# Kernel tuning notes

Hardware: AMD Instinct MI355X
Metric: run time of the kernel (lower is better)

Reference implementation:

```python
import jax, jax.numpy as jnp
import numpy as np

B, S, D = 2, 4096, 1024
H, DK, DV = 4, 128, 256          # head_k_dim, head_v_dim
KD, VD = H * DK, H * DV          # key_dim=512, value_dim=1024
RANK = 16                        # gate_low_rank_dim
GLN = 16.0                       # gate_logit_normalizer
EPS = 1e-5
C = 64                           # chunk size
NC = S // C


def setup_inputs() -> dict:
    key = jax.random.key(0)
    ks = jax.random.split(key, 9)
    w = lambda k, shape: (jax.random.normal(k, shape, jnp.float32) * 0.02)
    return {
        "x": jax.random.normal(ks[0], (B, S, D), jnp.float32),
        "Wq": w(ks[1], (D, KD)),
        "Wk": w(ks[2], (D, KD)),
        "Wv": w(ks[3], (D, VD)),
        "Wgk1": w(ks[4], (D, RANK)),
        "Wgk2": w(ks[5], (RANK, KD)),
        "bgk": jnp.zeros((KD,), jnp.float32),
        "Wg": w(ks[6], (D, VD)),
        "Wo": w(ks[7], (VD, D)),
        "norm_w": jnp.ones((DV,), jnp.float32),
    }


def _gla_chunk(q, k, v, gk):
    """Chunkwise gated linear attention. q,k,gk: [B,S,H,DK]; v: [B,S,H,DV]."""
    qc = q.reshape(B, NC, C, H, DK)
    kc = k.reshape(B, NC, C, H, DK)
    vc = v.reshape(B, NC, C, H, DV)
    gc = gk.reshape(B, NC, C, H, DK)
    gcum = jnp.cumsum(gc, axis=2)                       # inclusive within-chunk cumsum (<= 0)
    g_last = gcum[:, :, -1]                             # [B,NC,H,DK]
    q_t = qc * jnp.exp(gcum)                            # q decayed forward
    k_inv = kc * jnp.exp(-gcum)                         # for intra-chunk scores
    k_dec = kc * jnp.exp(g_last[:, :, None] - gcum)     # for state update (bounded)
    # intra-chunk causal scores
    A = jnp.einsum('bnthk,bnshk->bnhts', q_t, k_inv)    # [B,NC,H,C,C]
    mask = jnp.tril(jnp.ones((C, C), bool))
    A = jnp.where(mask, A, 0.0)
    o_intra = jnp.einsum('bnhts,bnshv->bnthv', A, vc)   # [B,NC,C,H,DV]
    # per-chunk state contribution
    kv = jnp.einsum('bnthk,bnthv->bnhkv', k_dec, vc)    # [B,NC,H,DK,DV]

    def step(state, inp):
        q_tc, gl, kvc = inp                             # [B,C,H,DK], [B,H,DK], [B,H,DK,DV]
        o_inter = jnp.einsum('bthk,bhkv->bthv', q_tc, state)
        state = state * jnp.exp(gl)[..., None] + kvc
        return state, o_inter

    xs = (jnp.swapaxes(q_t, 0, 1), jnp.swapaxes(g_last, 0, 1), jnp.swapaxes(kv, 0, 1))
    init = jnp.zeros((B, H, DK, DV), q.dtype)
    _, o_inter = jax.lax.scan(step, init, xs)           # [NC,B,C,H,DV]
    o = o_intra + jnp.swapaxes(o_inter, 0, 1)
    return o.reshape(B, S, H, DV)


def reference(x, Wq, Wk, Wv, Wgk1, Wgk2, bgk, Wg, Wo, norm_w):
    scale = DK ** -0.5
    q = (x @ Wq).reshape(B, S, H, DK) * scale
    k = (x @ Wk).reshape(B, S, H, DK)
    v = (x @ Wv).reshape(B, S, H, DV)
    gk = (jax.nn.log_sigmoid((x @ Wgk1) @ Wgk2 + bgk) / GLN).reshape(B, S, H, DK)
    o = _gla_chunk(q, k, v, gk)                          # [B,S,H,DV]
    # fused RMSNorm + swish gate (per-head norm over DV)
    g = (x @ Wg).reshape(B, S, H, DV)
    o = o * jax.lax.rsqrt(jnp.mean(o * o, axis=-1, keepdims=True) + EPS) * norm_w
    o = o * (g * jax.nn.sigmoid(g))
    return o.reshape(B, S, VD) @ Wo
```

## Files before the change

kernel.cpp:

```cpp
#include <hip/hip_runtime.h>

typedef __bf16 bf16_t;
typedef __bf16 bf16x8 __attribute__((ext_vector_type(8)));
typedef float  f32x4  __attribute__((ext_vector_type(4)));

#define MFMA16(a,b,c) __builtin_amdgcn_mfma_f32_16x16x32_bf16((a),(b),(c),0,0,0)

#define SCALE_Q 0.08838834764831845f

#define GLOBAL_LOAD_LDS16(gptr, lptr)                                          \
  __builtin_amdgcn_global_load_lds(                                            \
      (const __attribute__((address_space(1))) void*)(gptr),                   \
      (__attribute__((address_space(3))) void*)(lptr), 16, 0, 0)

__global__ __launch_bounds__(256) void k_convert(const void* __restrict__ src,
                                                 const unsigned int* __restrict__ nwp,
                                                 bf16_t* __restrict__ dst, int n) {
  bool isf32 = (nwp[0] == 0x3F800000u);
  int g = blockIdx.x * 256 + threadIdx.x;
  int i = g * 8;
  if (i >= n) return;
  if (isf32) {
    const float4* s = (const float4*)src;
    float4 a = s[g * 2], b = s[g * 2 + 1];
    bf16x8 o;
    o[0] = (bf16_t)a.x; o[1] = (bf16_t)a.y; o[2] = (bf16_t)a.z; o[3] = (bf16_t)a.w;
    o[4] = (bf16_t)b.x; o[5] = (bf16_t)b.y; o[6] = (bf16_t)b.z; o[7] = (bf16_t)b.w;
    *(bf16x8*)(dst + i) = o;
  } else {
    *(bf16x8*)(dst + i) = ((const bf16x8*)src)[g];
  }
}

struct ConvSrcs {
  const void *wq, *wk, *wv, *wg, *wo, *gk1, *gk2, *bgk, *nw;
};
__device__ __forceinline__ void convT_tile(const void* src, bf16_t* dst,
                                           int Ccols, int bx, int by,
                                           bool isf32, bf16_t (*t)[33]) {
  int tx = threadIdx.x & 31, ty = threadIdx.x >> 5;
  int r0 = by * 32, c0 = bx * 32;
#pragma unroll
  for (int i = 0; i < 4; i++) {
    int r = r0 + ty + i * 8, cc = c0 + tx;
    float v = isf32 ? ((const float*)src)[(size_t)r * Ccols + cc]
                    : (float)((const bf16_t*)src)[(size_t)r * Ccols + cc];
    t[ty + i * 8][tx] = (bf16_t)v;
  }
  __syncthreads();
#pragma unroll
  for (int i = 0; i < 4; i++) {
    int cc = c0 + ty + i * 8;
    dst[(size_t)cc * 1024 + r0 + tx] = t[tx][ty + i * 8];
  }
}
__device__ __forceinline__ void conv_straight(const void* src, bf16_t* dst,
                                              int base_blk, int n, bool isf32) {
  int g = (blockIdx.x - base_blk) * 256 + threadIdx.x;
  int i = g * 8;
  if (i >= n) return;
  if (isf32) {
    const float4* s = (const float4*)src;
    float4 a = s[g * 2], b = s[g * 2 + 1];
    bf16x8 o;
    o[0] = (bf16_t)a.x; o[1] = (bf16_t)a.y; o[2] = (bf16_t)a.z; o[3] = (bf16_t)a.w;
    o[4] = (bf16_t)b.x; o[5] = (bf16_t)b.y; o[6] = (bf16_t)b.z; o[7] = (bf16_t)b.w;
    *(bf16x8*)(dst + i) = o;
  } else {
    *(bf16x8*)(dst + i) = ((const bf16x8*)src)[g];
  }
}
__global__ __launch_bounds__(256) void k_convW(ConvSrcs s,
                                               const unsigned int* __restrict__ nwp,
                                               bf16_t* __restrict__ tWcat,
                                               bf16_t* __restrict__ tWo,
                                               bf16_t* __restrict__ cWgk1,
                                               bf16_t* __restrict__ cWgk2,
                                               bf16_t* __restrict__ cbgk,
                                               bf16_t* __restrict__ cnw) {
  __shared__ bf16_t t[32][33];
  bool isf32 = (nwp[0] == 0x3F800000u);
  int blk = blockIdx.x;
  if (blk < 512) {
    convT_tile(s.wq, tWcat, 512, blk & 15, blk >> 4, isf32, t);
  } else if (blk < 1024) {
    int b2 = blk - 512;
    convT_tile(s.wk, tWcat + (size_t)512 * 1024, 512, b2 & 15, b2 >> 4, isf32, t);
  } else if (blk < 2048) {
    int b2 = blk - 1024;
    convT_tile(s.wv, tWcat + (size_t)1024 * 1024, 1024, b2 & 31, b2 >> 5, isf32, t);
  } else if (blk < 3072) {
    int b2 = blk - 2048;
    convT_tile(s.wg, tWcat + (size_t)2048 * 1024, 1024, b2 & 31, b2 >> 5, isf32, t);
  } else if (blk < 4096) {
    int b2 = blk - 3072;
    convT_tile(s.wo, tWo, 1024, b2 & 31, b2 >> 5, isf32, t);
  } else if (blk < 4104) {
    conv_straight(s.gk1, cWgk1, 4096, 16384, isf32);
  } else if (blk < 4108) {
    conv_straight(s.gk2, cWgk2, 4104, 8192, isf32);
  } else if (blk == 4108) {
    conv_straight(s.bgk, cbgk, 4108, 512, isf32);
  } else {
    conv_straight(s.nw, cnw, 4109, 256, isf32);
  }
}

__global__ __launch_bounds__(256) void k_gk1(const bf16_t* __restrict__ x,
                                             const bf16_t* __restrict__ W1,
                                             float* __restrict__ tmp) {
  int wave = threadIdx.x >> 6, lane = threadIdx.x & 63;
  int m = blockIdx.x * 4 + wave;
  const bf16_t* xr = x + (size_t)m * 1024;
  float p[16];
#pragma unroll
  for (int n = 0; n < 16; n++) p[n] = 0.f;
  for (int kk = 0; kk < 16; kk++) {
    int k = kk * 64 + lane;
    float xv = (float)xr[k];
    bf16x8 w0 = *(const bf16x8*)(W1 + k * 16);
    bf16x8 w1 = *(const bf16x8*)(W1 + k * 16 + 8);
#pragma unroll
    for (int j = 0; j < 8; j++) {
      p[j]     += xv * (float)w0[j];
      p[8 + j] += xv * (float)w1[j];
    }
  }
#pragma unroll
  for (int off = 1; off < 64; off <<= 1) {
#pragma unroll
    for (int n = 0; n < 16; n++) p[n] += __shfl_xor(p[n], off, 64);
  }
#pragma unroll
  for (int n = 0; n < 16; n++)
    if (lane == n) tmp[(size_t)m * 16 + n] = p[n];
}

__global__ __launch_bounds__(256) void k_gk2(const float* __restrict__ tmp,
                                             const bf16_t* __restrict__ W2,
                                             const bf16_t* __restrict__ bgk,
                                             float* __restrict__ gcum) {
  int g = blockIdx.x * 256 + threadIdx.x;
  int m = g >> 6;
  int n0 = (g & 63) * 8;
  float acc[8];
#pragma unroll
  for (int j = 0; j < 8; j++) acc[j] = 0.f;
  for (int k = 0; k < 16; k++) {
    float tv = tmp[(size_t)m * 16 + k];
    bf16x8 w = *(const bf16x8*)(W2 + k * 512 + n0);
#pragma unroll
    for (int j = 0; j < 8; j++) acc[j] += tv * (float)w[j];
  }
  int b = m >> 12, s = m & 4095;
  int h = n0 >> 7, dk0 = n0 & 127;
  float* dst = gcum + (((size_t)(b * 4 + h) * 4096 + s) * 128 + dk0);
#pragma unroll
  for (int j = 0; j < 8; j++) {
    float z = acc[j] + (float)bgk[n0 + j];
    float lg = -__logf(1.f + __expf(-z)) * (1.f / 16.f);
    dst[j] = fmaxf(lg, -4.0f);
  }
}

__global__ __launch_bounds__(128) void k_cumsum(float* __restrict__ gcum,
                                                float* __restrict__ glast) {
  int blk = blockIdx.x;
  int dk = threadIdx.x;
  float* base = gcum + (size_t)blk * 8192;
  float run = 0.f;
  for (int t = 0; t < 64; t++) {
    run += base[t * 128 + dk];
    base[t * 128 + dk] = run;
  }
  glast[(size_t)blk * 128 + dk] = run;
}

__global__ __launch_bounds__(256, 4) void k_gemm(const bf16_t* __restrict__ Ag,
                                              const bf16_t* __restrict__ Bt,
                                              int mode,
                                              const float* __restrict__ gcum,
                                              const float* __restrict__ glast,
                                              bf16_t* __restrict__ qt,
                                              bf16_t* __restrict__ kinv,
                                              bf16_t* __restrict__ kdec,
                                              bf16_t* __restrict__ vr,
                                              bf16_t* __restrict__ gmat,
                                              float* __restrict__ fout) {
  __shared__ __attribute__((aligned(16))) bf16_t As[2 * 128 * 32];
  __shared__ __attribute__((aligned(16))) bf16_t Bs[2 * 128 * 32];
  int tid = threadIdx.x;
  int wave = tid >> 6, lane = tid & 63, quad = lane >> 4, c = lane & 15;
  int m0 = blockIdx.y * 128, n0 = blockIdx.x * 128;
  int wm = (wave >> 1) * 64, wn = (wave & 1) * 64;
  int r0s = wave * 32 + (lane >> 2);
  int r1s = r0s + 16;
  int s = lane & 3;
  int f0 = (s - (r0s >> 1)) & 3;
  int f1 = (s - (r1s >> 1)) & 3;
  const bf16_t* a0 = Ag + (size_t)(m0 + r0s) * 1024 + f0 * 8;
  const bf16_t* a1 = Ag + (size_t)(m0 + r1s) * 1024 + f1 * 8;
  const bf16_t* b0 = Bt + (size_t)(n0 + r0s) * 1024 + f0 * 8;
  const bf16_t* b1 = Bt + (size_t)(n0 + r1s) * 1024 + f1 * 8;
  bf16_t* lA = As + wave * 1024;
  bf16_t* lB = Bs + wave * 1024;
  int raOff[4], rbOff[4];
#pragma unroll
  for (int t4 = 0; t4 < 4; t4++) {
    int ra = wm + t4 * 16 + c;
    raOff[t4] = ra * 32 + (((quad + (ra >> 1)) & 3) * 8);
    int rb = wn + t4 * 16 + c;
    rbOff[t4] = rb * 32 + (((quad + (rb >> 1)) & 3) * 8);
  }
  GLOBAL_LOAD_LDS16(a0, lA);
  GLOBAL_LOAD_LDS16(a1, lA + 512);
  GLOBAL_LOAD_LDS16(b0, lB);
  GLOBAL_LOAD_LDS16(b1, lB + 512);
  f32x4 acc[4][4] = {};
  for (int k0 = 0; k0 < 1024; k0 += 32) {
    __syncthreads();
    int cur = (k0 >> 5) & 1;
    int nxtoff = (cur ^ 1) * 4096;
    if (k0 + 32 < 1024) {
      GLOBAL_LOAD_LDS16(a0 + k0 + 32, lA + nxtoff);
      GLOBAL_LOAD_LDS16(a1 + k0 + 32, lA + nxtoff + 512);
      GLOBAL_LOAD_LDS16(b0 + k0 + 32, lB + nxtoff);
      GLOBAL_LOAD_LDS16(b1 + k0 + 32, lB + nxtoff + 512);
    }
    int curoff = cur * 4096;
    bf16x8 af[4], bfr[4];
#pragma unroll
    for (int t4 = 0; t4 < 4; t4++) af[t4] = *(const bf16x8*)(As + curoff + raOff[t4]);
#pragma unroll
    for (int t4 = 0; t4 < 4; t4++) bfr[t4] = *(const bf16x8*)(Bs + curoff + rbOff[t4]);
#pragma unroll
    for (int mt = 0; mt < 4; mt++)
#pragma unroll
      for (int nt = 0; nt < 4; nt++)
        acc[mt][nt] = MFMA16(af[mt], bfr[nt], acc[mt][nt]);
  }
#pragma unroll
  for (int mt = 0; mt < 4; mt++)
#pragma unroll
    for (int nt = 0; nt < 4; nt++)
#pragma unroll
      for (int r = 0; r < 4; r++) {
        int m = m0 + wm + mt * 16 + quad * 4 + r;
        int n = n0 + wn + nt * 16 + c;
        float v = acc[mt][nt][r];
        if (mode == 1) {
          fout[(size_t)m * 1024 + n] = v;
        } else if (n0 < 512) {
          int b = m >> 12, ss = m & 4095, h = n >> 7, dk = n & 127;
          size_t idx = ((size_t)(b * 4 + h) * 4096 + ss) * 128 + dk;
          qt[idx] = (bf16_t)(v * SCALE_Q * __expf(gcum[idx]));
        } else if (n0 < 1024) {
          int nk = n - 512;
          int b = m >> 12, ss = m & 4095, h = nk >> 7, dk = nk & 127;
          size_t idx = ((size_t)(b * 4 + h) * 4096 + ss) * 128 + dk;
          float gc = gcum[idx];
          float gl = glast[((size_t)(b * 4 + h) * 64 + (ss >> 6)) * 128 + dk];
          kinv[idx] = (bf16_t)(v * __expf(fminf(-gc, 30.f)));
          kdec[idx] = (bf16_t)(v * __expf(gl - gc));
        } else if (n0 < 2048) {
          int nv = n - 1024;
          int b = m >> 12, ss = m & 4095, h = nv >> 8, dv = nv & 255;
          vr[((size_t)(b * 4 + h) * 4096 + ss) * 256 + dv] = (bf16_t)v;
        } else {
          gmat[(size_t)m * 1024 + (n - 2048)] = (bf16_t)v;
        }
      }
}

__global__ __launch_bounds__(256) void k_attA(const bf16_t* __restrict__ qt,
                                              const bf16_t* __restrict__ kinv,
                                              bf16_t* __restrict__ Aout) {
  int blk = blockIdx.x;
  size_t cb = (size_t)blk * 8192;
  int tid = threadIdx.x, wave = tid >> 6, lane = tid & 63;
  int quad = lane >> 4, c = lane & 15;
  f32x4 acc[4] = {};
  for (int kk = 0; kk < 128; kk += 32) {
    bf16x8 a = *(const bf16x8*)(qt + cb + (size_t)(wave * 16 + c) * 128 + kk + quad * 8);
#pragma unroll
    for (int nt = 0; nt < 4; nt++) {
      bf16x8 bb = *(const bf16x8*)(kinv + cb + (size_t)(nt * 16 + c) * 128 + kk + quad * 8);
      acc[nt] = MFMA16(a, bb, acc[nt]);
    }
  }
#pragma unroll
  for (int nt = 0; nt < 4; nt++)
#pragma unroll
    for (int r = 0; r < 4; r++) {
      int row = wave * 16 + quad * 4 + r, col = nt * 16 + c;
      Aout[(size_t)blk * 4096 + row * 64 + col] =
          (bf16_t)(col <= row ? acc[nt][r] : 0.f);
    }
}

__global__ __launch_bounds__(256, 3) void k_kv(const bf16_t* __restrict__ kdec,
                                            const bf16_t* __restrict__ vr,
                                            bf16_t* __restrict__ kv) {
  int blk = blockIdx.x;
  __shared__ __attribute__((aligned(16))) bf16_t ls_kd[64 * 128];
  __shared__ __attribute__((aligned(16))) bf16_t ls_v[64 * 256];
  int tid = threadIdx.x, wave = tid >> 6, lane = tid & 63;
  int quad = lane >> 4, c = lane & 15;
  size_t cb = (size_t)blk * 8192;
  size_t cv = (size_t)blk * 16384;
  size_t sb = (size_t)blk * 32768;
#pragma unroll
  for (int j = 0; j < 4; j++) {
    int idx = tid + j * 256;
    int row = idx >> 4, col = (idx & 15) * 8;
    *(bf16x8*)&ls_kd[row * 128 + col] = *(const bf16x8*)(kdec + cb + (size_t)row * 128 + col);
  }
#pragma unroll
  for (int j = 0; j < 8; j++) {
    int idx = tid + j * 256;
    int row = idx >> 5, col = (idx & 31) * 8;
    *(bf16x8*)&ls_v[row * 256 + col] = *(const bf16x8*)(vr + cv + (size_t)row * 256 + col);
  }
  __syncthreads();
  int kbase = (wave >> 1) * 64;
  for (int pos = 0; pos < 2; pos++) {
    int dvbase = (wave & 1) * 64 + pos * 128;
    f32x4 acc[4][4] = {};
    for (int kk = 0; kk < 64; kk += 32) {
      bf16x8 a[4], bb[4];
#pragma unroll
      for (int mt = 0; mt < 4; mt++)
#pragma unroll
        for (int j = 0; j < 8; j++)
          a[mt][j] = ls_kd[(kk + quad * 8 + j) * 128 + kbase + mt * 16 + c];
#pragma unroll
      for (int nt = 0; nt < 4; nt++)
#pragma unroll
        for (int j = 0; j < 8; j++)
          bb[nt][j] = ls_v[(kk + quad * 8 + j) * 256 + dvbase + nt * 16 + c];
#pragma unroll
      for (int mt = 0; mt < 4; mt++)
#pragma unroll
        for (int nt = 0; nt < 4; nt++)
          acc[mt][nt] = MFMA16(a[mt], bb[nt], acc[mt][nt]);
    }
#pragma unroll
    for (int mt = 0; mt < 4; mt++)
#pragma unroll
      for (int nt = 0; nt < 4; nt++)
#pragma unroll
        for (int r = 0; r < 4; r++) {
          int kg = kbase + mt * 16 + quad * 4 + r;
          int dg = dvbase + nt * 16 + c;
          kv[sb + (size_t)kg * 256 + dg] = (bf16_t)acc[mt][nt][r];
        }
  }
}

__global__ __launch_bounds__(256) void k_scan2(bf16_t* __restrict__ states,
                                               const float* __restrict__ glast) {
  int g = blockIdx.x * 256 + threadIdx.x;
  int bh = g >> 15;
  int idx = g & 32767;
  int kg = idx >> 8;
  bf16_t* p = states + (size_t)bh * 64 * 32768 + idx;
  const float* gl = glast + (size_t)bh * 64 * 128 + kg;
  float carry = 0.f;
#pragma unroll 4
  for (int n = 0; n < 64; n++) {
    float kvv = (float)p[(size_t)n * 32768];
    float e = __expf(gl[n * 128]);
    p[(size_t)n * 32768] = (bf16_t)carry;
    carry = carry * e + kvv;
  }
}

__global__ __launch_bounds__(256, 4) void k_o(const bf16_t* __restrict__ qt,
                                           const bf16_t* __restrict__ Amat,
                                           const bf16_t* __restrict__ vr,
                                           const bf16_t* __restrict__ states,
                                           const bf16_t* __restrict__ gmat,
                                           const bf16_t* __restrict__ normw,
                                           bf16_t* __restrict__ ob) {
  int blk = blockIdx.x;
  int bh = blk >> 6, n = blk & 63, b = bh >> 2, h = bh & 3;
  __shared__ __attribute__((aligned(16))) bf16_t ls[64 * 256];
  __shared__ __attribute__((aligned(16))) float lred[64][4];
  int tid = threadIdx.x, wave = tid >> 6, lane = tid & 63;
  int quad = lane >> 4, c = lane & 15;
  size_t cb = (size_t)blk * 8192;
  size_t cv = (size_t)blk * 16384;
  size_t sb = (size_t)blk * 32768;
  f32x4 acc[4][4] = {};
  for (int half = 0; half < 2; half++) {
    __syncthreads();
#pragma unroll
    for (int i = 0; i < 8; i++) {
      int idx = tid + i * 256;
      int row = idx >> 5, col = (idx & 31) * 8;
      *(bf16x8*)&ls[row * 256 + col] =
          *(const bf16x8*)(states + sb + (size_t)(half * 64 + row) * 256 + col);
    }
    __syncthreads();
    for (int kk2 = 0; kk2 < 2; kk2++) {
      int kl = kk2 * 32, kg = half * 64 + kl;
      bf16x8 a[4], bb[4];
#pragma unroll
      for (int mt = 0; mt < 4; mt++)
        a[mt] = *(const bf16x8*)(qt + cb + (size_t)(mt * 16 + c) * 128 + kg + quad * 8);
#pragma unroll
      for (int nt = 0; nt < 4; nt++)
#pragma unroll
        for (int j = 0; j < 8; j++)
          bb[nt][j] = ls[(kl + quad * 8 + j) * 256 + wave * 64 + nt * 16 + c];
#pragma unroll
      for (int mt = 0; mt < 4; mt++)
#pragma unroll
        for (int nt = 0; nt < 4; nt++)
          acc[mt][nt] = MFMA16(a[mt], bb[nt], acc[mt][nt]);
    }
  }
  __syncthreads();
#pragma unroll
  for (int i = 0; i < 8; i++) {
    int idx = tid + i * 256;
    int row = idx >> 5, col = (idx & 31) * 8;
    *(bf16x8*)&ls[row * 256 + col] =
        *(const bf16x8*)(vr + cv + (size_t)row * 256 + col);
  }
  __syncthreads();
  for (int kk = 0; kk < 64; kk += 32) {
    bf16x8 a[4], bb[4];
#pragma unroll
    for (int mt = 0; mt < 4; mt++)
      a[mt] = *(const bf16x8*)(Amat + (size_t)blk * 4096 + (size_t)(mt * 16 + c) * 64 + kk + quad * 8);
#pragma unroll
    for (int nt = 0; nt < 4; nt++)
#pragma unroll
      for (int j = 0; j < 8; j++)
        bb[nt][j] = ls[(kk + quad * 8 + j) * 256 + wave * 64 + nt * 16 + c];
#pragma unroll
    for (int mt = 0; mt < 4; mt++)
#pragma unroll
      for (int nt = 0; nt < 4; nt++)
        acc[mt][nt] = MFMA16(a[mt], bb[nt], acc[mt][nt]);
  }
  float p[4][4];
#pragma unroll
  for (int mt = 0; mt < 4; mt++)
#pragma unroll
    for (int r = 0; r < 4; r++) {
      float s = 0.f;
#pragma unroll
      for (int nt = 0; nt < 4; nt++) s += acc[mt][nt][r] * acc[mt][nt][r];
      p[mt][r] = s;
    }
#pragma unroll
  for (int off = 1; off < 16; off <<= 1) {
#pragma unroll
    for (int mt = 0; mt < 4; mt++)
#pragma unroll
      for (int r = 0; r < 4; r++) p[mt][r] += __shfl_xor(p[mt][r], off, 64);
  }
  if (c == 0) {
#pragma unroll
    for (int mt = 0; mt < 4; mt++)
#pragma unroll
      for (int r = 0; r < 4; r++) lred[mt * 16 + quad * 4 + r][wave] = p[mt][r];
  }
  __syncthreads();
#pragma unroll
  for (int mt = 0; mt < 4; mt++)
#pragma unroll
    for (int r = 0; r < 4; r++) {
      int row = mt * 16 + quad * 4 + r;
      float tot = lred[row][0] + lred[row][1] + lred[row][2] + lred[row][3];
      float rs = rsqrtf(tot * (1.f / 256.f) + 1e-5f);
      int sg = n * 64 + row;
      size_t gb = ((size_t)(b * 4096 + sg)) * 1024 + h * 256;
#pragma unroll
      for (int nt = 0; nt < 4; nt++) {
        int dv = wave * 64 + nt * 16 + c;
        float ov = acc[mt][nt][r] * rs * (float)normw[dv];
        float gv = (float)gmat[gb + dv];
        ov *= gv / (1.f + __expf(-gv));
        ob[gb + dv] = (bf16_t)ov;
      }
    }
}

extern "C" void kernel_launch(void* const* d_in, const int* in_sizes, int n_in,
                              void* d_out, int out_size, void* d_ws, size_t ws_size,
                              hipStream_t stream) {
  (void)in_sizes; (void)n_in; (void)out_size; (void)ws_size;
  const unsigned int* nw_oracle = (const unsigned int*)d_in[9];

  char* ws = (char*)d_ws;
  size_t off = 0;
  auto alloc = [&](size_t bytes) -> void* {
    void* p = ws + off;
    off += (bytes + 255) & ~(size_t)255;
    return p;
  };
  bf16_t* states = (bf16_t*)alloc((size_t)512 * 32768 * 2);
  bf16_t* cx     = states;
  float*  glast  = (float*) alloc((size_t)8 * 64 * 128 * 4);
  float*  tmp    = (float*) alloc((size_t)8192 * 16 * 4);
  float*  gcum   = (float*) alloc((size_t)8 * 4096 * 128 * 4);
  bf16_t* ob     = (bf16_t*)gcum;
  bf16_t* qt     = (bf16_t*)alloc((size_t)8 * 4096 * 128 * 2);
  bf16_t* kinv   = (bf16_t*)alloc((size_t)8 * 4096 * 128 * 2);
  bf16_t* kdec   = (bf16_t*)alloc((size_t)8 * 4096 * 128 * 2);
  bf16_t* vr     = (bf16_t*)alloc((size_t)8 * 4096 * 256 * 2);
  bf16_t* gmat   = (bf16_t*)alloc((size_t)8192 * 1024 * 2);
  bf16_t* Amat   = (bf16_t*)alloc((size_t)512 * 4096 * 2);
  bf16_t* tWcat  = (bf16_t*)alloc((size_t)3072 * 1024 * 2);
  bf16_t* cWgk1  = (bf16_t*)alloc((size_t)1024 * 16 * 2);
  bf16_t* cWgk2  = (bf16_t*)alloc((size_t)16 * 512 * 2);
  bf16_t* cbgk   = (bf16_t*)alloc((size_t)512 * 2);
  bf16_t* tWo    = (bf16_t*)alloc((size_t)1024 * 1024 * 2);
  bf16_t* cnw    = (bf16_t*)alloc((size_t)256 * 2);

  k_convert<<<4096, 256, 0, stream>>>(d_in[0], nw_oracle, cx, 8192 * 1024);
  ConvSrcs cs{d_in[1], d_in[2], d_in[3], d_in[7], d_in[8],
              d_in[4], d_in[5], d_in[6], d_in[9]};
  k_convW<<<4110, 256, 0, stream>>>(cs, nw_oracle, tWcat, tWo,
                                    cWgk1, cWgk2, cbgk, cnw);

  k_gk1<<<2048, 256, 0, stream>>>(cx, cWgk1, tmp);
  k_gk2<<<2048, 256, 0, stream>>>(tmp, cWgk2, cbgk, gcum);
  k_cumsum<<<512, 128, 0, stream>>>(gcum, glast);
  k_gemm<<<dim3(24, 64), 256, 0, stream>>>(cx, tWcat, 0, gcum, glast,
                                           qt, kinv, kdec, vr, gmat, nullptr);
  k_attA<<<512, 256, 0, stream>>>(qt, kinv, Amat);
  k_kv<<<512, 256, 0, stream>>>(kdec, vr, states);
  k_scan2<<<1024, 256, 0, stream>>>(states, glast);
  k_o<<<512, 256, 0, stream>>>(qt, Amat, vr, states, gmat, cnw, ob);
  k_gemm<<<dim3(8, 64), 256, 0, stream>>>(ob, tWo, 1, nullptr, nullptr,
                                          nullptr, nullptr, nullptr, nullptr, nullptr,
                                          (float*)d_out);
}
```

Measured before the change: 343.2 us.

## Rewrite projection GEMMs with larger tiles, 512 threads, XOR-swizzled LDS and grid swizzle

Replaces the 128x128, 256-thread GEMM with a templated kernel that uses 256x256 (or 128x256) tiles, 8 waves, a K-step of 64 with XOR-swizzled LDS, and explicit vmcnt waits with barriers for double buffering. It also remaps the block index for L2 locality and raises wave priority during MFMA. The aim is more data reuse per LDS load and fewer global loads per FLOP. In exchange it needs up to 128KB of dynamic shared memory and launches fewer blocks (384 and 256), which may underfill the CUs.

```diff
diff --git a/kernel.cpp b/kernel.cpp
--- a/kernel.cpp
+++ b/kernel.cpp
@@ -12,6 +12,9 @@
   __builtin_amdgcn_global_load_lds(                                            \
       (const __attribute__((address_space(1))) void*)(gptr),                   \
       (__attribute__((address_space(3))) void*)(lptr), 16, 0, 0)
+
+#define SBAR   __builtin_amdgcn_s_barrier()
+#define SCHEDB __builtin_amdgcn_sched_barrier(0)
 
 __global__ __launch_bounds__(256) void k_convert(const void* __restrict__ src,
                                                  const unsigned int* __restrict__ nwp,
@@ -176,98 +179,134 @@
   glast[(size_t)blk * 128 + dk] = run;
 }
 
-__global__ __launch_bounds__(256, 4) void k_gemm(const bf16_t* __restrict__ Ag,
-                                              const bf16_t* __restrict__ Bt,
-                                              int mode,
-                                              const float* __restrict__ gcum,
-                                              const float* __restrict__ glast,
-                                              bf16_t* __restrict__ qt,
-                                              bf16_t* __restrict__ kinv,
-                                              bf16_t* __restrict__ kdec,
-                                              bf16_t* __restrict__ vr,
-                                              bf16_t* __restrict__ gmat,
-                                              float* __restrict__ fout) {
-  __shared__ __attribute__((aligned(16))) bf16_t As[2 * 128 * 32];
-  __shared__ __attribute__((aligned(16))) bf16_t Bs[2 * 128 * 32];
+template <int BM, int BN, int NBN, int MODE>
+__global__ __launch_bounds__(512, 2) void k_gemm2(
+    const bf16_t* __restrict__ Ag, const bf16_t* __restrict__ Bt,
+    const float* __restrict__ gcum, const float* __restrict__ glast,
+    bf16_t* __restrict__ qt, bf16_t* __restrict__ kinv,
+    bf16_t* __restrict__ kdec, bf16_t* __restrict__ vr,
+    bf16_t* __restrict__ gmat, float* __restrict__ fout) {
+  constexpr int MT = BM / 2 / 16;
+  constexpr int ALDS = BM * 64;
+  constexpr int BLDS = BN * 64;
+  constexpr int NT = 16;
+  extern __shared__ __attribute__((aligned(16))) bf16_t sm[];
+  bf16_t* As = sm;
+  bf16_t* Bs = sm + 2 * ALDS;
+
   int tid = threadIdx.x;
-  int wave = tid >> 6, lane = tid & 63, quad = lane >> 4, c = lane & 15;
-  int m0 = blockIdx.y * 128, n0 = blockIdx.x * 128;
-  int wm = (wave >> 1) * 64, wn = (wave & 1) * 64;
-  int r0s = wave * 32 + (lane >> 2);
-  int r1s = r0s + 16;
-  int s = lane & 3;
-  int f0 = (s - (r0s >> 1)) & 3;
-  int f1 = (s - (r1s >> 1)) & 3;
-  const bf16_t* a0 = Ag + (size_t)(m0 + r0s) * 1024 + f0 * 8;
-  const bf16_t* a1 = Ag + (size_t)(m0 + r1s) * 1024 + f1 * 8;
-  const bf16_t* b0 = Bt + (size_t)(n0 + r0s) * 1024 + f0 * 8;
-  const bf16_t* b1 = Bt + (size_t)(n0 + r1s) * 1024 + f1 * 8;
-  bf16_t* lA = As + wave * 1024;
-  bf16_t* lB = Bs + wave * 1024;
-  int raOff[4], rbOff[4];
-#pragma unroll
-  for (int t4 = 0; t4 < 4; t4++) {
-    int ra = wm + t4 * 16 + c;
-    raOff[t4] = ra * 32 + (((quad + (ra >> 1)) & 3) * 8);
-    int rb = wn + t4 * 16 + c;
-    rbOff[t4] = rb * 32 + (((quad + (rb >> 1)) & 3) * 8);
-  }
-  GLOBAL_LOAD_LDS16(a0, lA);
-  GLOBAL_LOAD_LDS16(a1, lA + 512);
-  GLOBAL_LOAD_LDS16(b0, lB);
-  GLOBAL_LOAD_LDS16(b1, lB + 512);
-  f32x4 acc[4][4] = {};
-  for (int k0 = 0; k0 < 1024; k0 += 32) {
-    __syncthreads();
-    int cur = (k0 >> 5) & 1;
-    int nxtoff = (cur ^ 1) * 4096;
-    if (k0 + 32 < 1024) {
-      GLOBAL_LOAD_LDS16(a0 + k0 + 32, lA + nxtoff);
-      GLOBAL_LOAD_LDS16(a1 + k0 + 32, lA + nxtoff + 512);
-      GLOBAL_LOAD_LDS16(b0 + k0 + 32, lB + nxtoff);
-      GLOBAL_LOAD_LDS16(b1 + k0 + 32, lB + nxtoff + 512);
-    }
-    int curoff = cur * 4096;
-    bf16x8 af[4], bfr[4];
-#pragma unroll
-    for (int t4 = 0; t4 < 4; t4++) af[t4] = *(const bf16x8*)(As + curoff + raOff[t4]);
-#pragma unroll
-    for (int t4 = 0; t4 < 4; t4++) bfr[t4] = *(const bf16x8*)(Bs + curoff + rbOff[t4]);
-#pragma unroll
-    for (int mt = 0; mt < 4; mt++)
+  int w = tid >> 6, lane = tid & 63;
+  int WM = w >> 2, WN = w & 3;
+  int quad = lane >> 4, c = lane & 15;
+
+  int nblk = gridDim.x;
+  int bid = blockIdx.x;
+  int swz = (bid & 7) * (nblk >> 3) + (bid >> 3);
+  int bm = swz / NBN, bn = swz % NBN;
+  int m0 = bm * BM, n0 = bn * BN;
+
+  int srow = w * 8 + (lane >> 3);
+  int scol = ((lane & 7) ^ (lane >> 3)) * 8;
+  const bf16_t* aBase = Ag + (size_t)(m0 + srow) * 1024 + scol;
+  const bf16_t* bBase = Bt + (size_t)(n0 + srow) * 1024 + scol;
+
+  auto stage = [&](int t, int buf) {
+    int kof = t * 64;
+#pragma unroll
+    for (int j = 0; j < BM / 64; j++)
+      GLOBAL_LOAD_LDS16(aBase + (size_t)j * 64 * 1024 + kof,
+                        As + buf * ALDS + j * 4096 + w * 512);
+#pragma unroll
+    for (int j = 0; j < BN / 64; j++)
+      GLOBAL_LOAD_LDS16(bBase + (size_t)j * 64 * 1024 + kof,
+                        Bs + buf * BLDS + j * 4096 + w * 512);
+  };
+
+  int sx = c & 7;
+  int aRowOff[MT], bRowOff[4];
+#pragma unroll
+  for (int mt = 0; mt < MT; mt++) aRowOff[mt] = (WM * (BM / 2) + mt * 16 + c) * 64;
+#pragma unroll
+  for (int nt = 0; nt < 4; nt++) bRowOff[nt] = (WN * 64 + nt * 16 + c) * 64;
+
+  f32x4 acc[MT][4] = {};
+
+  stage(0, 0);
+  stage(1, 1);
+
+  auto compute = [&](int buf) {
+#pragma unroll
+    for (int ks = 0; ks < 2; ks++) {
+      int so = (((ks << 2) | quad) ^ sx) << 3;
+      bf16x8 bfr[4];
 #pragma unroll
       for (int nt = 0; nt < 4; nt++)
-        acc[mt][nt] = MFMA16(af[mt], bfr[nt], acc[mt][nt]);
-  }
-#pragma unroll
-  for (int mt = 0; mt < 4; mt++)
+        bfr[nt] = *(const bf16x8*)(Bs + buf * BLDS + bRowOff[nt] + so);
+#pragma unroll
+      for (int mt = 0; mt < MT; mt++) {
+        bf16x8 af = *(const bf16x8*)(As + buf * ALDS + aRowOff[mt] + so);
+#pragma unroll
+        for (int nt = 0; nt < 4; nt++)
+          acc[mt][nt] = MFMA16(af, bfr[nt], acc[mt][nt]);
+      }
+    }
+  };
+
+#pragma unroll 2
+  for (int t = 0; t < NT; t++) {
+    if (t < NT - 1) {
+      if constexpr (BM == 256)
+        asm volatile("s_waitcnt vmcnt(8)" ::: "memory");
+      else
+        asm volatile("s_waitcnt vmcnt(6)" ::: "memory");
+    } else {
+      asm volatile("s_waitcnt vmcnt(0)" ::: "memory");
+    }
+    SCHEDB;
+    SBAR;
+    SCHEDB;
+    __builtin_amdgcn_s_setprio(1);
+    compute(t & 1);
+    __builtin_amdgcn_s_setprio(0);
+    SCHEDB;
+    SBAR;
+    SCHEDB;
+    if (t + 2 < NT) stage(t + 2, t & 1);
+  }
+
+  int mwb = m0 + WM * (BM / 2);
+  int nwb = n0 + WN * 64;
+#pragma unroll
+  for (int mt = 0; mt < MT; mt++)
 #pragma unroll
     for (int nt = 0; nt < 4; nt++)
 #pragma unroll
       for (int r = 0; r < 4; r++) {
-        int m = m0 + wm + mt * 16 + quad * 4 + r;
-        int n = n0 + wn + nt * 16 + c;
+        int m = mwb + mt * 16 + quad * 4 + r;
+        int n = nwb + nt * 16 + c;
         float v = acc[mt][nt][r];
-        if (mode == 1) {
+        if constexpr (MODE == 1) {
           fout[(size_t)m * 1024 + n] = v;
-        } else if (n0 < 512) {
-          int b = m >> 12, ss = m & 4095, h = n >> 7, dk = n & 127;
-          size_t idx = ((size_t)(b * 4 + h) * 4096 + ss) * 128 + dk;
-          qt[idx] = (bf16_t)(v * SCALE_Q * __expf(gcum[idx]));
-        } else if (n0 < 1024) {
-          int nk = n - 512;
-          int b = m >> 12, ss = m & 4095, h = nk >> 7, dk = nk & 127;
-          size_t idx = ((size_t)(b * 4 + h) * 4096 + ss) * 128 + dk;
-          float gc = gcum[idx];
-          float gl = glast[((size_t)(b * 4 + h) * 64 + (ss >> 6)) * 128 + dk];
-          kinv[idx] = (bf16_t)(v * __expf(fminf(-gc, 30.f)));
-          kdec[idx] = (bf16_t)(v * __expf(gl - gc));
-        } else if (n0 < 2048) {
-          int nv = n - 1024;
-          int b = m >> 12, ss = m & 4095, h = nv >> 8, dv = nv & 255;
-          vr[((size_t)(b * 4 + h) * 4096 + ss) * 256 + dv] = (bf16_t)v;
         } else {
-          gmat[(size_t)m * 1024 + (n - 2048)] = (bf16_t)v;
+          if (n0 < 512) {
+            int b = m >> 12, ss = m & 4095, h = n >> 7, dk = n & 127;
+            size_t idx = ((size_t)(b * 4 + h) * 4096 + ss) * 128 + dk;
+            qt[idx] = (bf16_t)(v * SCALE_Q * __expf(gcum[idx]));
+          } else if (n0 < 1024) {
+            int nk = n - 512;
+            int b = m >> 12, ss = m & 4095, h = nk >> 7, dk = nk & 127;
+            size_t idx = ((size_t)(b * 4 + h) * 4096 + ss) * 128 + dk;
+            float gc = gcum[idx];
+            float gl = glast[((size_t)(b * 4 + h) * 64 + (ss >> 6)) * 128 + dk];
+            kinv[idx] = (bf16_t)(v * __expf(fminf(-gc, 30.f)));
+            kdec[idx] = (bf16_t)(v * __expf(gl - gc));
+          } else if (n0 < 2048) {
+            int nv = n - 1024;
+            int b = m >> 12, ss = m & 4095, h = nv >> 8, dv = nv & 255;
+            vr[((size_t)(b * 4 + h) * 4096 + ss) * 256 + dv] = (bf16_t)v;
+          } else {
+            gmat[(size_t)m * 1024 + (n - 2048)] = (bf16_t)v;
+          }
         }
       }
 }
@@ -494,6 +533,15 @@
                               hipStream_t stream) {
   (void)in_sizes; (void)n_in; (void)out_size; (void)ws_size;
   const unsigned int* nw_oracle = (const unsigned int*)d_in[9];
+
+  static int attr_done = 0;
+  if (!attr_done) {
+    (void)hipFuncSetAttribute((const void*)&k_gemm2<256, 256, 12, 0>,
+                              hipFuncAttributeMaxDynamicSharedMemorySize, 131072);
+    (void)hipFuncSetAttribute((const void*)&k_gemm2<128, 256, 4, 1>,
+                              hipFuncAttributeMaxDynamicSharedMemorySize, 98304);
+    attr_done = 1;
+  }
 
   char* ws = (char*)d_ws;
   size_t off = 0;
@@ -530,13 +578,13 @@
   k_gk1<<<2048, 256, 0, stream>>>(cx, cWgk1, tmp);
   k_gk2<<<2048, 256, 0, stream>>>(tmp, cWgk2, cbgk, gcum);
   k_cumsum<<<512, 128, 0, stream>>>(gcum, glast);
-  k_gemm<<<dim3(24, 64), 256, 0, stream>>>(cx, tWcat, 0, gcum, glast,
-                                           qt, kinv, kdec, vr, gmat, nullptr);
+  k_gemm2<256, 256, 12, 0><<<384, 512, 131072, stream>>>(
+      cx, tWcat, gcum, glast, qt, kinv, kdec, vr, gmat, nullptr);
   k_attA<<<512, 256, 0, stream>>>(qt, kinv, Amat);
   k_kv<<<512, 256, 0, stream>>>(kdec, vr, states);
   k_scan2<<<1024, 256, 0, stream>>>(states, glast);
   k_o<<<512, 256, 0, stream>>>(qt, Amat, vr, states, gmat, cnw, ob);
-  k_gemm<<<dim3(8, 64), 256, 0, stream>>>(ob, tWo, 1, nullptr, nullptr,
-                                          nullptr, nullptr, nullptr, nullptr, nullptr,
-                                          (float*)d_out);
-}
+  k_gemm2<128, 256, 4, 1><<<256, 512, 98304, stream>>>(
+      ob, tWo, nullptr, nullptr, nullptr, nullptr, nullptr, nullptr, nullptr,
+      (float*)d_out);
+}
```

New measurement: 349.3 us. About the same (+1.8%).

## Fuse gate projection with cumsum and fold intra-chunk scores into output kernel

Applied to the files above, without the earlier changes.

Merges the second low-rank gate projection, log-sigmoid and chunk cumsum into one kernel, so gcum is written once instead of written then read and rewritten. It also computes the masked intra-chunk score matrix inside the output kernel and keeps it in an XOR-swizzled LDS buffer, which drops the separate attention-score kernel and its global round trip. The cost is more LDS per block in the output kernel, with its occupancy bound lowered from 4 to 3 blocks, and less parallelism in the gate kernel.

```diff
diff --git a/kernel.cpp b/kernel.cpp
--- a/kernel.cpp
+++ b/kernel.cpp
@@ -136,42 +136,36 @@
     if (lane == n) tmp[(size_t)m * 16 + n] = p[n];
 }
 
-__global__ __launch_bounds__(256) void k_gk2(const float* __restrict__ tmp,
-                                             const bf16_t* __restrict__ W2,
-                                             const bf16_t* __restrict__ bgk,
-                                             float* __restrict__ gcum) {
-  int g = blockIdx.x * 256 + threadIdx.x;
-  int m = g >> 6;
-  int n0 = (g & 63) * 8;
-  float acc[8];
-#pragma unroll
-  for (int j = 0; j < 8; j++) acc[j] = 0.f;
-  for (int k = 0; k < 16; k++) {
-    float tv = tmp[(size_t)m * 16 + k];
-    bf16x8 w = *(const bf16x8*)(W2 + k * 512 + n0);
-#pragma unroll
-    for (int j = 0; j < 8; j++) acc[j] += tv * (float)w[j];
-  }
-  int b = m >> 12, s = m & 4095;
-  int h = n0 >> 7, dk0 = n0 & 127;
-  float* dst = gcum + (((size_t)(b * 4 + h) * 4096 + s) * 128 + dk0);
-#pragma unroll
-  for (int j = 0; j < 8; j++) {
-    float z = acc[j] + (float)bgk[n0 + j];
+__global__ __launch_bounds__(128) void k_gkcum(const float* __restrict__ tmp,
+                                               const bf16_t* __restrict__ W2,
+                                               const bf16_t* __restrict__ bgk,
+                                               float* __restrict__ gcum,
+                                               float* __restrict__ glast) {
+  __shared__ float lt[64][16];
+  int blk = blockIdx.x;
+  int bh = blk >> 6, n = blk & 63;
+  int b = bh >> 2, h = bh & 3;
+  int dk = threadIdx.x;
+  int m0 = b * 4096 + n * 64;
+  const float4* tsrc = (const float4*)(tmp + (size_t)m0 * 16);
+  ((float4*)lt)[dk * 2]     = tsrc[dk * 2];
+  ((float4*)lt)[dk * 2 + 1] = tsrc[dk * 2 + 1];
+  int col = h * 128 + dk;
+  float wv[16];
+#pragma unroll
+  for (int k = 0; k < 16; k++) wv[k] = (float)W2[k * 512 + col];
+  float bv = (float)bgk[col];
+  __syncthreads();
+  float run = 0.f;
+  float* dst = gcum + ((size_t)bh * 4096 + (size_t)n * 64) * 128 + dk;
+  for (int t = 0; t < 64; t++) {
+    float acc = 0.f;
+#pragma unroll
+    for (int k = 0; k < 16; k++) acc += lt[t][k] * wv[k];
+    float z = acc + bv;
     float lg = -__logf(1.f + __expf(-z)) * (1.f / 16.f);
-    dst[j] = fmaxf(lg, -4.0f);
-  }
-}
-
-__global__ __launch_bounds__(128) void k_cumsum(float* __restrict__ gcum,
-                                                float* __restrict__ glast) {
-  int blk = blockIdx.x;
-  int dk = threadIdx.x;
-  float* base = gcum + (size_t)blk * 8192;
-  float run = 0.f;
-  for (int t = 0; t < 64; t++) {
-    run += base[t * 128 + dk];
-    base[t * 128 + dk] = run;
+    run += fmaxf(lg, -4.0f);
+    dst[t * 128] = run;
   }
   glast[(size_t)blk * 128 + dk] = run;
 }
@@ -272,32 +266,6 @@
       }
 }
 
-__global__ __launch_bounds__(256) void k_attA(const bf16_t* __restrict__ qt,
-                                              const bf16_t* __restrict__ kinv,
-                                              bf16_t* __restrict__ Aout) {
-  int blk = blockIdx.x;
-  size_t cb = (size_t)blk * 8192;
-  int tid = threadIdx.x, wave = tid >> 6, lane = tid & 63;
-  int quad = lane >> 4, c = lane & 15;
-  f32x4 acc[4] = {};
-  for (int kk = 0; kk < 128; kk += 32) {
-    bf16x8 a = *(const bf16x8*)(qt + cb + (size_t)(wave * 16 + c) * 128 + kk + quad * 8);
-#pragma unroll
-    for (int nt = 0; nt < 4; nt++) {
-      bf16x8 bb = *(const bf16x8*)(kinv + cb + (size_t)(nt * 16 + c) * 128 + kk + quad * 8);
-      acc[nt] = MFMA16(a, bb, acc[nt]);
-    }
-  }
-#pragma unroll
-  for (int nt = 0; nt < 4; nt++)
-#pragma unroll
-    for (int r = 0; r < 4; r++) {
-      int row = wave * 16 + quad * 4 + r, col = nt * 16 + c;
-      Aout[(size_t)blk * 4096 + row * 64 + col] =
-          (bf16_t)(col <= row ? acc[nt][r] : 0.f);
-    }
-}
-
 __global__ __launch_bounds__(256, 3) void k_kv(const bf16_t* __restrict__ kdec,
                                             const bf16_t* __restrict__ vr,
                                             bf16_t* __restrict__ kv) {
@@ -375,15 +343,16 @@
   }
 }
 
-__global__ __launch_bounds__(256, 4) void k_o(const bf16_t* __restrict__ qt,
-                                           const bf16_t* __restrict__ Amat,
-                                           const bf16_t* __restrict__ vr,
-                                           const bf16_t* __restrict__ states,
-                                           const bf16_t* __restrict__ gmat,
-                                           const bf16_t* __restrict__ normw,
-                                           bf16_t* __restrict__ ob) {
+__global__ __launch_bounds__(256, 3) void k_o2(const bf16_t* __restrict__ qt,
+                                               const bf16_t* __restrict__ kinv,
+                                               const bf16_t* __restrict__ vr,
+                                               const bf16_t* __restrict__ states,
+                                               const bf16_t* __restrict__ gmat,
+                                               const bf16_t* __restrict__ normw,
+                                               bf16_t* __restrict__ ob) {
   int blk = blockIdx.x;
   int bh = blk >> 6, n = blk & 63, b = bh >> 2, h = bh & 3;
+  __shared__ __attribute__((aligned(16))) bf16_t As[64 * 64];
   __shared__ __attribute__((aligned(16))) bf16_t ls[64 * 256];
   __shared__ __attribute__((aligned(16))) float lred[64][4];
   int tid = threadIdx.x, wave = tid >> 6, lane = tid & 63;
@@ -391,6 +360,27 @@
   size_t cb = (size_t)blk * 8192;
   size_t cv = (size_t)blk * 16384;
   size_t sb = (size_t)blk * 32768;
+
+  {
+    f32x4 a4[4] = {};
+    for (int kk = 0; kk < 128; kk += 32) {
+      bf16x8 a = *(const bf16x8*)(qt + cb + (size_t)(wave * 16 + c) * 128 + kk + quad * 8);
+#pragma unroll
+      for (int nt = 0; nt < 4; nt++) {
+        bf16x8 bb = *(const bf16x8*)(kinv + cb + (size_t)(nt * 16 + c) * 128 + kk + quad * 8);
+        a4[nt] = MFMA16(a, bb, a4[nt]);
+      }
+    }
+#pragma unroll
+    for (int nt = 0; nt < 4; nt++)
+#pragma unroll
+      for (int r = 0; r < 4; r++) {
+        int row = wave * 16 + quad * 4 + r, col = nt * 16 + c;
+        As[row * 64 + (col ^ ((row & 7) * 8))] =
+            (bf16_t)(col <= row ? a4[nt][r] : 0.f);
+      }
+  }
+
   f32x4 acc[4][4] = {};
   for (int half = 0; half < 2; half++) {
     __syncthreads();
@@ -429,11 +419,12 @@
         *(const bf16x8*)(vr + cv + (size_t)row * 256 + col);
   }
   __syncthreads();
+  int akey = (c & 7) * 8;
   for (int kk = 0; kk < 64; kk += 32) {
     bf16x8 a[4], bb[4];
 #pragma unroll
     for (int mt = 0; mt < 4; mt++)
-      a[mt] = *(const bf16x8*)(Amat + (size_t)blk * 4096 + (size_t)(mt * 16 + c) * 64 + kk + quad * 8);
+      a[mt] = *(const bf16x8*)&As[(mt * 16 + c) * 64 + ((kk + quad * 8) ^ akey)];
 #pragma unroll
     for (int nt = 0; nt < 4; nt++)
 #pragma unroll
@@ -513,7 +504,6 @@
   bf16_t* kdec   = (bf16_t*)alloc((size_t)8 * 4096 * 128 * 2);
   bf16_t* vr     = (bf16_t*)alloc((size_t)8 * 4096 * 256 * 2);
   bf16_t* gmat   = (bf16_t*)alloc((size_t)8192 * 1024 * 2);
-  bf16_t* Amat   = (bf16_t*)alloc((size_t)512 * 4096 * 2);
   bf16_t* tWcat  = (bf16_t*)alloc((size_t)3072 * 1024 * 2);
   bf16_t* cWgk1  = (bf16_t*)alloc((size_t)1024 * 16 * 2);
   bf16_t* cWgk2  = (bf16_t*)alloc((size_t)16 * 512 * 2);
@@ -528,14 +518,12 @@
                                     cWgk1, cWgk2, cbgk, cnw);
 
   k_gk1<<<2048, 256, 0, stream>>>(cx, cWgk1, tmp);
-  k_gk2<<<2048, 256, 0, stream>>>(tmp, cWgk2, cbgk, gcum);
-  k_cumsum<<<512, 128, 0, stream>>>(gcum, glast);
+  k_gkcum<<<512, 128, 0, stream>>>(tmp, cWgk2, cbgk, gcum, glast);
   k_gemm<<<dim3(24, 64), 256, 0, stream>>>(cx, tWcat, 0, gcum, glast,
                                            qt, kinv, kdec, vr, gmat, nullptr);
-  k_attA<<<512, 256, 0, stream>>>(qt, kinv, Amat);
   k_kv<<<512, 256, 0, stream>>>(kdec, vr, states);
   k_scan2<<<1024, 256, 0, stream>>>(states, glast);
-  k_o<<<512, 256, 0, stream>>>(qt, Amat, vr, states, gmat, cnw, ob);
+  k_o2<<<512, 256, 0, stream>>>(qt, kinv, vr, states, gmat, cnw, ob);
   k_gemm<<<dim3(8, 64), 256, 0, stream>>>(ob, tWo, 1, nullptr, nullptr,
                                           nullptr, nullptr, nullptr, nullptr, nullptr,
                                           (float*)d_out);
```

New measurement: 321.2 us. -6.4%, faster.
